# Kernel optimization log

Measured on AMD Instinct MI355X. Metric: run time of the kernel, lower is better.

## Reference

```python
import jax, jax.numpy as jnp
import numpy as np

B, T, C, H = 4096, 4, 1024, 8
DH = C // H
SCALE = DH ** -0.5
LN_EPS = 1e-5


def setup_inputs() -> dict:
    key = jax.random.key(0)
    k1, k2, k3 = jax.random.split(key, 3)
    feats = jax.random.normal(k1, (B, T, C), dtype=jnp.float32)
    Wqkv = jax.random.normal(k2, (T, C, 3 * C), dtype=jnp.float32) * 0.02
    bqkv = jnp.zeros((T, 3 * C), dtype=jnp.float32)
    Wproj = jax.random.normal(k3, (T, C, C), dtype=jnp.float32) * 0.02
    bproj = jnp.zeros((T, C), dtype=jnp.float32)
    gamma = jnp.ones((C,), dtype=jnp.float32)
    beta = jnp.zeros((C,), dtype=jnp.float32)
    return {"feats": feats, "Wqkv": Wqkv, "bqkv": bqkv,
            "Wproj": Wproj, "bproj": bproj, "gamma": gamma, "beta": beta}


def reference(feats, Wqkv, bqkv, Wproj, bproj, gamma, beta):
    # Grouped per-task QKV projection: [B,T,C] x [T,C,3C] -> [B,T,3C]
    qkv = jnp.einsum('btc,tcd->btd', feats, Wqkv) + bqkv
    q, k, v = jnp.split(qkv, 3, axis=-1)           # each [B,T,C]
    q = q.reshape(B, T, H, DH)
    k = k.reshape(B, T, H, DH)
    v = v.reshape(B, T, H, DH)
    # Cross-task attention: scores[b, query_task, key_task, head]
    scores = jnp.einsum('bqhd,bkhd->bqkh', q, k) * SCALE
    attn = jax.nn.softmax(scores, axis=2)          # softmax over key-task dim
    ctx = jnp.einsum('bqkh,bkhd->bqhd', attn, v)   # [B,T,H,DH]
    ctx = ctx.reshape(B, T, C)
    # Grouped per-task output projection (dropout is identity in eval)
    ctx = jnp.einsum('btc,tcd->btd', ctx, Wproj) + bproj
    # Residual + shared LayerNorm over channel dim
    x = ctx + feats
    mu = jnp.mean(x, axis=-1, keepdims=True)
    var = jnp.mean(jnp.square(x - mu), axis=-1, keepdims=True)
    return (x - mu) * jax.lax.rsqrt(var + LN_EPS) * gamma + beta
```

## Files before the change

kernel.cpp:

```cpp
#include <hip/hip_runtime.h>
#include <hip/hip_bf16.h>
#include <cstdint>
#include <cstddef>

#define B_SZ 4096
#define T_SZ 4
#define C_SZ 1024
#define H_SZ 8
#define DH_SZ 128
#define NQKV 3072
#define SCALE_F 0.08838834764831845f

typedef float f32x4 __attribute__((ext_vector_type(4)));
typedef short s16x8 __attribute__((ext_vector_type(8)));

static __device__ __forceinline__ float bf2f(unsigned short u) {
    union { unsigned int i; float f; } x; x.i = ((unsigned int)u) << 16; return x.f;
}
static __device__ __forceinline__ unsigned short f2bf(float f) {
    union { unsigned int i; float f; } x; x.f = f;
    unsigned int r = x.i + 0x7FFFu + ((x.i >> 16) & 1u);
    return (unsigned short)(r >> 16);
}

typedef const __attribute__((address_space(1))) void* gas_ptr;
typedef __attribute__((address_space(3))) void* las_ptr;
static __device__ __forceinline__ void async16(const void* g, void* l) {
    __builtin_amdgcn_global_load_lds((gas_ptr)g, (las_ptr)l, 16, 0, 0);
}

__global__ __launch_bounds__(256) void cvt_f32_bf16(const float* __restrict__ src,
                                                    unsigned short* __restrict__ dst, int n4) {
    int i = blockIdx.x * 256 + threadIdx.x;
    if (i >= n4) return;
    float4 v = reinterpret_cast<const float4*>(src)[i];
    ushort4 o;
    o.x = f2bf(v.x); o.y = f2bf(v.y); o.z = f2bf(v.z); o.w = f2bf(v.w);
    reinterpret_cast<ushort4*>(dst)[i] = o;
}

__global__ __launch_bounds__(256) void transpose_cvt(const float* __restrict__ src,
                                                     unsigned short* __restrict__ dst,
                                                     int K, int N) {
    __shared__ float tile[32][33];
    const float* s = src + (size_t)blockIdx.z * K * N;
    unsigned short* d = dst + (size_t)blockIdx.z * K * N;
    int n0 = blockIdx.x * 32, k0 = blockIdx.y * 32;
    int tx = threadIdx.x, ty = threadIdx.y;
#pragma unroll
    for (int i = 0; i < 4; i++) {
        int k = k0 + ty + i * 8;
        tile[ty + i * 8][tx] = s[(size_t)k * N + n0 + tx];
    }
    __syncthreads();
#pragma unroll
    for (int i = 0; i < 4; i++) {
        int n = n0 + ty + i * 8;
        d[(size_t)n * K + k0 + tx] = f2bf(tile[tx][ty + i * 8]);
    }
}

template<int NSIZE, int EPI>
__global__ __launch_bounds__(512, 1) void gemm256(
    const unsigned short* __restrict__ A,
    const unsigned short* __restrict__ Bt,
    const float* __restrict__ bias,
    const float* __restrict__ resid,
    unsigned short* __restrict__ out_bf,
    float* __restrict__ out_f)
{
    constexpr int BK  = 64;
    constexpr int NT  = C_SZ / BK;
    constexpr int NBX = NSIZE / 256;
    constexpr int NBY = B_SZ / 256;
    constexpr int NWG = NBX * NBY * T_SZ;

    __shared__ __align__(16) unsigned short lds[65536];

    const int bid = blockIdx.x;
    const int swz = (bid & 7) * (NWG >> 3) + (bid >> 3);
    const int by  = swz & (NBY - 1);
    const int tmp = swz >> 4;
    const int bx  = tmp % NBX;
    const int t   = tmp / NBX;
    const int m0  = by * 256;
    const int n0  = bx * 256;

    const int tid  = threadIdx.x;
    const int lane = tid & 63;
    const int w    = tid >> 6;
    const int wm   = w >> 2;
    const int wn   = w & 3;
    const int quad = lane >> 4;
    const int l16  = lane & 15;

    const int q0  = w * 128 + lane;
    const int q1  = q0 + 64;
    const int r0  = q0 >> 3, ch0 = (q0 & 7) ^ (r0 & 7);
    const int r1  = q1 >> 3, ch1 = (q1 & 7) ^ (r1 & 7);
    const unsigned short* Abase = A + (size_t)t * C_SZ;
    const unsigned short* Bbase = Bt + (size_t)t * NSIZE * C_SZ;
    const unsigned short* gA0 = Abase + (size_t)(m0 + r0) * (T_SZ * C_SZ) + ch0 * 8;
    const unsigned short* gA1 = Abase + (size_t)(m0 + r1) * (T_SZ * C_SZ) + ch1 * 8;
    const unsigned short* gB0 = Bbase + (size_t)(n0 + r0) * C_SZ + ch0 * 8;
    const unsigned short* gB1 = Bbase + (size_t)(n0 + r1) * C_SZ + ch1 * 8;
    unsigned short* dA0 = &lds[(w * 2 + 0) * 512];
    unsigned short* dA1 = &lds[(w * 2 + 1) * 512];
    unsigned short* dB0 = &lds[32768 + (w * 2 + 0) * 512];
    unsigned short* dB1 = &lds[32768 + (w * 2 + 1) * 512];

#define STG_A(buf, h, kt) do { \
    async16(gA0 + (size_t)(h) * 128 * (T_SZ * C_SZ) + (kt) * BK, dA0 + (buf) * 16384 + (h) * 8192); \
    async16(gA1 + (size_t)(h) * 128 * (T_SZ * C_SZ) + (kt) * BK, dA1 + (buf) * 16384 + (h) * 8192); \
} while (0)
#define STG_B(buf, h, kt) do { \
    async16(gB0 + (size_t)(h) * 128 * C_SZ + (kt) * BK, dB0 + (buf) * 16384 + (h) * 8192); \
    async16(gB1 + (size_t)(h) * 128 * C_SZ + (kt) * BK, dB1 + (buf) * 16384 + (h) * 8192); \
} while (0)

    const int s7   = l16 & 7;
    const int swk0 = ((0 * 4 + quad) ^ s7) * 8;
    const int swk1 = ((1 * 4 + quad) ^ s7) * 8;
    const unsigned short* aR = &lds[wm * 8192 + l16 * 64];
    const unsigned short* bR = &lds[32768 + (wn >> 1) * 8192 + ((wn & 1) * 64 + l16) * 64];

#define LD_A(buf, mh) do { \
    _Pragma("unroll") \
    for (int mi = 0; mi < 4; ++mi) { \
        af[mi][0] = *(const s16x8*)(aR + (buf) * 16384 + ((mh) * 4 + mi) * 1024 + swk0); \
        af[mi][1] = *(const s16x8*)(aR + (buf) * 16384 + ((mh) * 4 + mi) * 1024 + swk1); \
    } \
} while (0)
#define LD_B(buf, nh, dst) do { \
    _Pragma("unroll") \
    for (int ni = 0; ni < 2; ++ni) { \
        dst[ni][0] = *(const s16x8*)(bR + (buf) * 16384 + ((nh) * 2 + ni) * 1024 + swk0); \
        dst[ni][1] = *(const s16x8*)(bR + (buf) * 16384 + ((nh) * 2 + ni) * 1024 + swk1); \
    } \
} while (0)
#define MM(mh, nh, bsrc) do { \
    _Pragma("unroll") \
    for (int mi = 0; mi < 4; ++mi) \
    _Pragma("unroll") \
    for (int ni = 0; ni < 2; ++ni) { \
        acc[(mh) * 4 + mi][(nh) * 2 + ni] = __builtin_amdgcn_mfma_f32_16x16x32_bf16( \
            af[mi][0], bsrc[ni][0], acc[(mh) * 4 + mi][(nh) * 2 + ni], 0, 0, 0); \
        acc[(mh) * 4 + mi][(nh) * 2 + ni] = __builtin_amdgcn_mfma_f32_16x16x32_bf16( \
            af[mi][1], bsrc[ni][1], acc[(mh) * 4 + mi][(nh) * 2 + ni], 0, 0, 0); \
    } \
} while (0)
#define WAITK() do { \
    asm volatile("s_waitcnt lgkmcnt(0)"); \
    __builtin_amdgcn_sched_barrier(0); \
} while (0)
#define KTILE(buf, kt, SP0, SP23, VMC) do { \
     \
    asm volatile("s_waitcnt vmcnt(" #VMC ")"); \
    __builtin_amdgcn_sched_barrier(0); \
    LD_A(buf, 0); LD_B(buf, 0, bq0); \
    if (SP0) STG_A((buf) ^ 1, 1, (kt) + 1); \
    __builtin_amdgcn_s_barrier(); \
    WAITK(); \
    __builtin_amdgcn_s_setprio(1); MM(0, 0, bq0); __builtin_amdgcn_s_setprio(0); \
    __builtin_amdgcn_s_barrier(); \
     \
    LD_B(buf, 1, bq1); \
    __builtin_amdgcn_s_barrier(); \
    WAITK(); \
    __builtin_amdgcn_s_setprio(1); MM(0, 1, bq1); __builtin_amdgcn_s_setprio(0); \
    __builtin_amdgcn_s_barrier(); \
     \
    LD_A(buf, 1); \
    if (SP23) { STG_B(buf, 0, (kt) + 2); STG_B(buf, 1, (kt) + 2); } \
    __builtin_amdgcn_s_barrier(); \
    WAITK(); \
    __builtin_amdgcn_s_setprio(1); MM(1, 1, bq1); __builtin_amdgcn_s_setprio(0); \
    __builtin_amdgcn_s_barrier(); \
     \
    if (SP23) STG_A(buf, 0, (kt) + 2); \
    __builtin_amdgcn_s_barrier(); \
    WAITK(); \
    __builtin_amdgcn_s_setprio(1); MM(1, 0, bq0); __builtin_amdgcn_s_setprio(0); \
    __builtin_amdgcn_s_barrier(); \
} while (0)

    f32x4 acc[8][4] = {};
    s16x8 af[4][2], bq0[2][2], bq1[2][2];

    STG_B(0, 0, 0); STG_B(0, 1, 0); STG_A(0, 0, 0); STG_A(0, 1, 0);
    STG_B(1, 0, 1); STG_B(1, 1, 1); STG_A(1, 0, 1);
    asm volatile("s_waitcnt vmcnt(6)");
    __builtin_amdgcn_sched_barrier(0);
    __builtin_amdgcn_s_barrier();

#pragma clang loop unroll(disable)
    for (int it = 0; it < 7; ++it) {
        int kt = it * 2;
        KTILE(0, kt, 1, 1, 6);
        KTILE(1, kt + 1, 1, 1, 6);
    }
    KTILE(0, 14, 1, 0, 6);
    KTILE(1, 15, 0, 0, 0);

#undef KTILE
#undef WAITK
#undef MM
#undef LD_B
#undef LD_A
#undef STG_B
#undef STG_A

#pragma unroll
    for (int ni = 0; ni < 4; ++ni) {
        int gn = n0 + wn * 64 + ni * 16 + l16;
        float bi = bias[t * NSIZE + gn];
#pragma unroll
        for (int mi = 0; mi < 8; ++mi) {
#pragma unroll
            for (int r = 0; r < 4; ++r) {
                int gm = m0 + wm * 128 + mi * 16 + quad * 4 + r;
                size_t o = (size_t)(gm * T_SZ + t) * NSIZE + gn;
                float v = acc[mi][ni][r] + bi;
                if (EPI == 0) {
                    out_bf[o] = f2bf(v);
                } else {
                    out_f[o] = v + resid[o];
                }
            }
        }
    }
}

__global__ __launch_bounds__(256) void attn_kernel(const unsigned short* __restrict__ qkv,
                                                   unsigned short* __restrict__ ctx) {
    int wave = threadIdx.x >> 6, lane = threadIdx.x & 63;
    int g = blockIdx.x * 4 + wave;
    int b = g >> 3, h = g & 7;
    int d0 = lane * 2;

    const unsigned short* base = qkv + (size_t)b * T_SZ * NQKV + h * DH_SZ + d0;
    float qf[4][2], kf[4][2], vf[4][2];
#pragma unroll
    for (int i = 0; i < 4; i++) {
        const unsigned short* p = base + (size_t)i * NQKV;
        qf[i][0] = bf2f(p[0]);          qf[i][1] = bf2f(p[1]);
        kf[i][0] = bf2f(p[C_SZ]);       kf[i][1] = bf2f(p[C_SZ + 1]);
        vf[i][0] = bf2f(p[2 * C_SZ]);   vf[i][1] = bf2f(p[2 * C_SZ + 1]);
    }
    float s[4][4];
#pragma unroll
    for (int i = 0; i < 4; i++)
#pragma unroll
        for (int j = 0; j < 4; j++) {
            float p = qf[i][0] * kf[j][0] + qf[i][1] * kf[j][1];
#pragma unroll
            for (int off = 32; off > 0; off >>= 1) p += __shfl_xor(p, off);
            s[i][j] = p * SCALE_F;
        }
#pragma unroll
    for (int i = 0; i < 4; i++) {
        float m = fmaxf(fmaxf(s[i][0], s[i][1]), fmaxf(s[i][2], s[i][3]));
        float e0 = __expf(s[i][0] - m), e1 = __expf(s[i][1] - m);
        float e2 = __expf(s[i][2] - m), e3 = __expf(s[i][3] - m);
        float inv = 1.0f / (e0 + e1 + e2 + e3);
        s[i][0] = e0 * inv; s[i][1] = e1 * inv; s[i][2] = e2 * inv; s[i][3] = e3 * inv;
    }
#pragma unroll
    for (int i = 0; i < 4; i++) {
        float o0 = s[i][0] * vf[0][0] + s[i][1] * vf[1][0] + s[i][2] * vf[2][0] + s[i][3] * vf[3][0];
        float o1 = s[i][0] * vf[0][1] + s[i][1] * vf[1][1] + s[i][2] * vf[2][1] + s[i][3] * vf[3][1];
        size_t o = (size_t)(b * T_SZ + i) * C_SZ + h * DH_SZ + d0;
        ctx[o] = f2bf(o0); ctx[o + 1] = f2bf(o1);
    }
}

__global__ __launch_bounds__(256) void ln_kernel(const float* __restrict__ y,
                                                 const float* __restrict__ gamma,
                                                 const float* __restrict__ beta,
                                                 float* __restrict__ out) {
    int row = blockIdx.x;
    int lane = threadIdx.x & 63, wave = threadIdx.x >> 6;
    float4 v = reinterpret_cast<const float4*>(y + (size_t)row * C_SZ)[threadIdx.x];
    float s  = v.x + v.y + v.z + v.w;
    float ss = v.x * v.x + v.y * v.y + v.z * v.z + v.w * v.w;
#pragma unroll
    for (int off = 32; off > 0; off >>= 1) { s += __shfl_xor(s, off); ss += __shfl_xor(ss, off); }
    __shared__ float red[8];
    if (lane == 0) { red[wave] = s; red[wave + 4] = ss; }
    __syncthreads();
    float S  = red[0] + red[1] + red[2] + red[3];
    float SS = red[4] + red[5] + red[6] + red[7];
    float mean = S * (1.0f / C_SZ);
    float var  = SS * (1.0f / C_SZ) - mean * mean;
    float inv  = rsqrtf(var + 1e-5f);
    float4 g  = reinterpret_cast<const float4*>(gamma)[threadIdx.x];
    float4 be = reinterpret_cast<const float4*>(beta)[threadIdx.x];
    float4 o;
    o.x = (v.x - mean) * inv * g.x + be.x;
    o.y = (v.y - mean) * inv * g.y + be.y;
    o.z = (v.z - mean) * inv * g.z + be.z;
    o.w = (v.w - mean) * inv * g.w + be.w;
    reinterpret_cast<float4*>(out + (size_t)row * C_SZ)[threadIdx.x] = o;
}

extern "C" void kernel_launch(void* const* d_in, const int* in_sizes, int n_in,
                              void* d_out, int out_size, void* d_ws, size_t ws_size,
                              hipStream_t stream) {
    const float* feats = (const float*)d_in[0];
    const float* Wqkv  = (const float*)d_in[1];
    const float* bqkv  = (const float*)d_in[2];
    const float* Wproj = (const float*)d_in[3];
    const float* bproj = (const float*)d_in[4];
    const float* gamma = (const float*)d_in[5];
    const float* beta  = (const float*)d_in[6];
    float* out = (float*)d_out;

    char* ws = (char*)d_ws;
    unsigned short* feats_bf = (unsigned short*)(ws);
    unsigned short* wqkv_t   = (unsigned short*)(ws + 33554432);
    unsigned short* wproj_t  = (unsigned short*)(ws + 58720256);
    unsigned short* qkv      = (unsigned short*)(ws + 67108864);
    unsigned short* ctx      = (unsigned short*)(ws + 167772160);
    float* ybuf              = (float*)(ws + 67108864);

    cvt_f32_bf16<<<16384, 256, 0, stream>>>(feats, feats_bf, (B_SZ * T_SZ * C_SZ) / 4);
    transpose_cvt<<<dim3(96, 32, 4), dim3(32, 8), 0, stream>>>(Wqkv, wqkv_t, C_SZ, NQKV);
    transpose_cvt<<<dim3(32, 32, 4), dim3(32, 8), 0, stream>>>(Wproj, wproj_t, C_SZ, C_SZ);

    gemm256<NQKV, 0><<<dim3(768), 512, 0, stream>>>(
        feats_bf, wqkv_t, bqkv, nullptr, qkv, nullptr);

    attn_kernel<<<(B_SZ * H_SZ) / 4, 256, 0, stream>>>(qkv, ctx);

    gemm256<C_SZ, 1><<<dim3(256), 512, 0, stream>>>(
        ctx, wproj_t, bproj, feats, nullptr, ybuf);

    ln_kernel<<<B_SZ * T_SZ, 256, 0, stream>>>(ybuf, gamma, beta, out);
}
```

Before: 425.7 us.

## Halve GEMM pipeline barriers and vectorize attention with 16 lanes per head

The GEMM k-tile macro drops from two workgroup barriers per phase to one. It also removes the prologue wait/barrier and the redundant final LDS wait, cutting synchronization stalls between MFMA phases. The attention kernel now handles each (batch, head) with 16 lanes doing 128-bit bf16 loads and stores, instead of a full wave doing 2-element scalar accesses. This also shortens the shuffle reductions. Fewer barriers risk LDS read/write races between double-buffered stages if any hazard was relying on the removed syncs.

```diff
diff --git a/kernel.cpp b/kernel.cpp
--- a/kernel.cpp
+++ b/kernel.cpp
@@ -70,7 +70,6 @@
     float* __restrict__ out_f)
 {
     constexpr int BK  = 64;
-    constexpr int NT  = C_SZ / BK;
     constexpr int NBX = NSIZE / 256;
     constexpr int NBY = B_SZ / 256;
     constexpr int NWG = NBX * NBY * T_SZ;
@@ -157,31 +156,26 @@
      \
     asm volatile("s_waitcnt vmcnt(" #VMC ")"); \
     __builtin_amdgcn_sched_barrier(0); \
+    __builtin_amdgcn_s_barrier(); \
     LD_A(buf, 0); LD_B(buf, 0, bq0); \
     if (SP0) STG_A((buf) ^ 1, 1, (kt) + 1); \
-    __builtin_amdgcn_s_barrier(); \
     WAITK(); \
     __builtin_amdgcn_s_setprio(1); MM(0, 0, bq0); __builtin_amdgcn_s_setprio(0); \
+     \
     __builtin_amdgcn_s_barrier(); \
-     \
     LD_B(buf, 1, bq1); \
-    __builtin_amdgcn_s_barrier(); \
     WAITK(); \
     __builtin_amdgcn_s_setprio(1); MM(0, 1, bq1); __builtin_amdgcn_s_setprio(0); \
+     \
     __builtin_amdgcn_s_barrier(); \
-     \
     LD_A(buf, 1); \
     if (SP23) { STG_B(buf, 0, (kt) + 2); STG_B(buf, 1, (kt) + 2); } \
-    __builtin_amdgcn_s_barrier(); \
     WAITK(); \
     __builtin_amdgcn_s_setprio(1); MM(1, 1, bq1); __builtin_amdgcn_s_setprio(0); \
+     \
     __builtin_amdgcn_s_barrier(); \
-     \
     if (SP23) STG_A(buf, 0, (kt) + 2); \
-    __builtin_amdgcn_s_barrier(); \
-    WAITK(); \
     __builtin_amdgcn_s_setprio(1); MM(1, 0, bq0); __builtin_amdgcn_s_setprio(0); \
-    __builtin_amdgcn_s_barrier(); \
 } while (0)
 
     f32x4 acc[8][4] = {};
@@ -189,9 +183,6 @@
 
     STG_B(0, 0, 0); STG_B(0, 1, 0); STG_A(0, 0, 0); STG_A(0, 1, 0);
     STG_B(1, 0, 1); STG_B(1, 1, 1); STG_A(1, 0, 1);
-    asm volatile("s_waitcnt vmcnt(6)");
-    __builtin_amdgcn_sched_barrier(0);
-    __builtin_amdgcn_s_barrier();
 
 #pragma clang loop unroll(disable)
     for (int it = 0; it < 7; ++it) {
@@ -233,28 +224,39 @@
 
 __global__ __launch_bounds__(256) void attn_kernel(const unsigned short* __restrict__ qkv,
                                                    unsigned short* __restrict__ ctx) {
-    int wave = threadIdx.x >> 6, lane = threadIdx.x & 63;
-    int g = blockIdx.x * 4 + wave;
-    int b = g >> 3, h = g & 7;
-    int d0 = lane * 2;
-
-    const unsigned short* base = qkv + (size_t)b * T_SZ * NQKV + h * DH_SZ + d0;
-    float qf[4][2], kf[4][2], vf[4][2];
+    const int tid = threadIdx.x;
+    const int li  = tid & 15;
+    const int g   = blockIdx.x * 16 + (tid >> 4);
+    const int b   = g >> 3, h = g & 7;
+    const int d0  = li * 8;
+
+    const unsigned short* base = qkv + (size_t)b * (T_SZ * NQKV) + h * DH_SZ + d0;
+    float qf[4][8], kf[4][8], vf[4][8];
 #pragma unroll
     for (int i = 0; i < 4; i++) {
         const unsigned short* p = base + (size_t)i * NQKV;
-        qf[i][0] = bf2f(p[0]);          qf[i][1] = bf2f(p[1]);
-        kf[i][0] = bf2f(p[C_SZ]);       kf[i][1] = bf2f(p[C_SZ + 1]);
-        vf[i][0] = bf2f(p[2 * C_SZ]);   vf[i][1] = bf2f(p[2 * C_SZ + 1]);
+        s16x8 qv = *reinterpret_cast<const s16x8*>(p);
+        s16x8 kv = *reinterpret_cast<const s16x8*>(p + C_SZ);
+        s16x8 vv = *reinterpret_cast<const s16x8*>(p + 2 * C_SZ);
+#pragma unroll
+        for (int e = 0; e < 8; e++) {
+            qf[i][e] = bf2f((unsigned short)qv[e]);
+            kf[i][e] = bf2f((unsigned short)kv[e]);
+            vf[i][e] = bf2f((unsigned short)vv[e]);
+        }
     }
     float s[4][4];
 #pragma unroll
     for (int i = 0; i < 4; i++)
 #pragma unroll
         for (int j = 0; j < 4; j++) {
-            float p = qf[i][0] * kf[j][0] + qf[i][1] * kf[j][1];
-#pragma unroll
-            for (int off = 32; off > 0; off >>= 1) p += __shfl_xor(p, off);
+            float p = 0.0f;
+#pragma unroll
+            for (int e = 0; e < 8; e++) p += qf[i][e] * kf[j][e];
+            p += __shfl_xor(p, 8);
+            p += __shfl_xor(p, 4);
+            p += __shfl_xor(p, 2);
+            p += __shfl_xor(p, 1);
             s[i][j] = p * SCALE_F;
         }
 #pragma unroll
@@ -267,10 +269,14 @@
     }
 #pragma unroll
     for (int i = 0; i < 4; i++) {
-        float o0 = s[i][0] * vf[0][0] + s[i][1] * vf[1][0] + s[i][2] * vf[2][0] + s[i][3] * vf[3][0];
-        float o1 = s[i][0] * vf[0][1] + s[i][1] * vf[1][1] + s[i][2] * vf[2][1] + s[i][3] * vf[3][1];
-        size_t o = (size_t)(b * T_SZ + i) * C_SZ + h * DH_SZ + d0;
-        ctx[o] = f2bf(o0); ctx[o + 1] = f2bf(o1);
+        s16x8 ov;
+#pragma unroll
+        for (int e = 0; e < 8; e++) {
+            float o = s[i][0] * vf[0][e] + s[i][1] * vf[1][e]
+                    + s[i][2] * vf[2][e] + s[i][3] * vf[3][e];
+            ov[e] = (short)f2bf(o);
+        }
+        *reinterpret_cast<s16x8*>(ctx + (size_t)(b * T_SZ + i) * C_SZ + h * DH_SZ + d0) = ov;
     }
 }
 
@@ -330,7 +336,7 @@
     gemm256<NQKV, 0><<<dim3(768), 512, 0, stream>>>(
         feats_bf, wqkv_t, bqkv, nullptr, qkv, nullptr);
 
-    attn_kernel<<<(B_SZ * H_SZ) / 4, 256, 0, stream>>>(qkv, ctx);
+    attn_kernel<<<(B_SZ * H_SZ) / 16, 256, 0, stream>>>(qkv, ctx);
 
     gemm256<C_SZ, 1><<<dim3(256), 512, 0, stream>>>(
         ctx, wproj_t, bproj, feats, nullptr, ybuf);
```

Result: no change. 417.8 us (-1.9%).
